# Kernel optimization log

Hardware: AMD Instinct MI355X
Metric: run time of the kernel (lower is better)

## Reference

```python
import jax, jax.numpy as jnp
import numpy as np
import math

B, N, DIM = 8, 4096, 768
H, D = 12, 64
STAGES = 3
LN_EPS = 1e-5

def _ln(x, g, b):
    mu = jnp.mean(x, axis=-1, keepdims=True)
    var = jnp.mean(jnp.square(x - mu), axis=-1, keepdims=True)
    return (x - mu) * jax.lax.rsqrt(var + LN_EPS) * g + b

def _mlp(x, W, b, g, be):
    return jax.nn.gelu(_ln(x @ W + b, g, be), approximate=False)

def setup_inputs() -> dict:
    key = jax.random.key(0)
    ks = jax.random.split(key, 16)
    s = lambda i, shape, sc: jax.random.normal(ks[i], shape, jnp.float32) * sc
    return {
        "x": s(0, (B, N, DIM), 1.0),
        "Wq": s(1, (DIM, H * D), DIM ** -0.5),
        "Wk": s(2, (DIM, H * D), DIM ** -0.5),
        "Wv": s(3, (DIM, H * D), DIM ** -0.5),
        "pool_W": s(4, (STAGES, D, D), D ** -0.5),
        "pool_b": jnp.zeros((STAGES, D), jnp.float32),
        "pool_g": jnp.ones((STAGES, D), jnp.float32),
        "pool_be": jnp.zeros((STAGES, D), jnp.float32),
        "exp_W": s(5, (STAGES, D, D), D ** -0.5),
        "exp_b": jnp.zeros((STAGES, D), jnp.float32),
        "exp_g": jnp.ones((STAGES, D), jnp.float32),
        "exp_be": jnp.zeros((STAGES, D), jnp.float32),
        "Wo": s(6, (H * D, DIM), (H * D) ** -0.5),
        "bo": jnp.zeros((DIM,), jnp.float32),
    }

def reference(x, Wq, Wk, Wv, pool_W, pool_b, pool_g, pool_be,
              exp_W, exp_b, exp_g, exp_be, Wo, bo):
    b, n, _ = x.shape
    # project and split heads -> (b, h, n, d)
    def heads(y):
        return y.reshape(b, n, H, D).transpose(0, 2, 1, 3)
    q = heads(x @ Wq)
    k = heads(x @ Wk)
    v = heads(x @ Wv)
    fmap = lambda t: jax.nn.elu(t) + 1.0
    q = fmap(q)
    k = fmap(k)

    kc, vc = k, v
    for i in range(STAGES):
        s = kc.shape[2]
        if s > 1:
            pad = (-s) % 2
            if pad:
                kc = jnp.pad(kc, ((0, 0), (0, 0), (0, pad), (0, 0)))
                vc = jnp.pad(vc, ((0, 0), (0, 0), (0, pad), (0, 0)))
            kc = kc.reshape(b, H, -1, 2, D).mean(axis=3)
            kc = _mlp(kc, pool_W[i], pool_b[i], pool_g[i], pool_be[i])
            vc = vc.reshape(b, H, -1, 2, D).mean(axis=3)

    kc = kc / math.sqrt(kc.shape[2])
    kv = jnp.einsum('bhnd,bhne->bhde', kc, vc)       # (b,h,d,d)
    out = jnp.einsum('bhnd,bhde->bhne', q, kv)       # (b,h,n,d)
    k_sum = kc.sum(axis=2, keepdims=True)            # (b,h,1,d)
    q_k_sum = jnp.sum(q * k_sum, axis=-1, keepdims=True)  # (b,h,n,1)
    out = out / (q_k_sum + 1e-6)

    for i in reversed(range(STAGES)):
        out = _mlp(out, exp_W[i], exp_b[i], exp_g[i], exp_be[i])

    out = out.transpose(0, 2, 1, 3).reshape(b, n, H * D)
    return out @ Wo + bo
```

## Files before the change

kernel.cpp:

```cpp
#include <hip/hip_runtime.h>
#include <math.h>

#define B_   8
#define N_   4096
#define DIM_ 768
#define H_   12
#define D_   64

typedef unsigned short ushort_t;
typedef unsigned int uint_t;
typedef __attribute__((ext_vector_type(8))) short short8;
typedef __attribute__((ext_vector_type(4))) float f32x4;

__device__ __forceinline__ float gelu_exact(float z) {
  const float ax = fabsf(z) * 0.70710678118654752440f;
  const float t  = __builtin_amdgcn_rcpf(1.f + 0.3275911f * ax);
  float poly = ((((1.061405429f * t - 1.453152027f) * t + 1.421413741f) * t
                 - 0.284496736f) * t + 0.254829592f) * t;
  const float erfax = 1.f - poly * __expf(-ax * ax);
  const float erfv = __builtin_copysignf(erfax, z);
  return 0.5f * z * (1.f + erfv);
}

__device__ __forceinline__ ushort_t f2bf(float f) {
  union { float f; unsigned u; } x; x.f = f;
  unsigned r = x.u + 0x7FFFu + ((x.u >> 16) & 1u);
  return (ushort_t)(r >> 16);
}

__device__ __forceinline__ float bf2f(ushort_t h) {
  union { unsigned u; float f; } x; x.u = ((unsigned)h) << 16;
  return x.f;
}

__device__ __forceinline__ void gl_lds16(const ushort_t* g, ushort_t* l) {
  __builtin_amdgcn_global_load_lds(
      (const __attribute__((address_space(1))) void*)g,
      (__attribute__((address_space(3))) void*)l, 16, 0, 0);
}

__global__ __launch_bounds__(256) void transpose_w_bf16(
    const float* __restrict__ src, ushort_t* __restrict__ dst)
{
  __shared__ float t[32][33];
  const int lx = threadIdx.x & 31, ly = threadIdx.x >> 5;
  const int bx = blockIdx.x * 32;
  const int by = blockIdx.y * 32;
  #pragma unroll
  for (int j = 0; j < 32; j += 8)
    t[ly + j][lx] = src[(size_t)(by + ly + j) * 768 + bx + lx];
  __syncthreads();
  #pragma unroll
  for (int j = 0; j < 32; j += 8)
    dst[(size_t)(bx + ly + j) * 768 + by + lx] = f2bf(t[lx][ly + j]);
}

__global__ __launch_bounds__(256) void transpose64_bf16(
    const float* __restrict__ pW, const float* __restrict__ eW,
    ushort_t* __restrict__ dst)
{
  const int m = blockIdx.x;
  const float* src = (m < 3) ? (pW + m * 4096) : (eW + (m - 3) * 4096);
  ushort_t* o = dst + m * 4096;
  for (int i = threadIdx.x; i < 4096; i += 256) {
    const int r = i >> 6, c = i & 63;
    o[c * 64 + r] = f2bf(src[r * 64 + c]);
  }
}

__global__ __launch_bounds__(256) void conv_f32_bf16(
    const float* __restrict__ src, ushort_t* __restrict__ dst)
{
  const int i = blockIdx.x * 256 + threadIdx.x;
  float4 f = ((const float4*)src)[i];
  ushort4 o;
  o.x = f2bf(f.x); o.y = f2bf(f.y); o.z = f2bf(f.z); o.w = f2bf(f.w);
  ((ushort4*)dst)[i] = o;
}

__global__ __launch_bounds__(256) void pool8_x(
    const ushort_t* __restrict__ xb, ushort_t* __restrict__ x8)
{
  const int idx = blockIdx.x * 256 + threadIdx.x;
  const int r = idx / 96, gc = idx - r * 96;
  const ushort_t* p = xb + (size_t)(8 * r) * 768 + gc * 8;
  float s[8] = {};
  #pragma unroll
  for (int j = 0; j < 8; ++j) {
    short8 v = *(const short8*)(p + (size_t)j * 768);
    #pragma unroll
    for (int e = 0; e < 8; ++e) s[e] += bf2f((ushort_t)v[e]);
  }
  short8 o;
  #pragma unroll
  for (int e = 0; e < 8; ++e) o[e] = (short)f2bf(0.125f * s[e]);
  *(short8*)(x8 + (size_t)r * 768 + gc * 8) = o;
}

#define GEMM_MAINLOOP(A, Bt, K)                                               \
  __shared__ ushort_t As[128 * 32];                                           \
  __shared__ ushort_t Bs[128 * 32];                                           \
  const int tid = threadIdx.x;                                                \
  const int nwg_ = (int)(gridDim.x * gridDim.y);                              \
  const int wgid0_ = (int)(blockIdx.y * gridDim.x + blockIdx.x);              \
  const int wgid_ = (wgid0_ & 7) * (nwg_ >> 3) + (wgid0_ >> 3);               \
  const int row0 = (wgid_ / (int)gridDim.x) * 128;                            \
  const int col0 = (wgid_ % (int)gridDim.x) * 128;                            \
  const int sr = tid >> 2;                                                    \
  const int sk = (tid & 3) * 8;                                               \
  const ushort_t* Ag0 = (A) + (size_t)(row0 + sr) * (K) + sk;                 \
  const ushort_t* Ag1 = Ag0 + (size_t)64 * (K);                               \
  const ushort_t* Bg0 = (Bt) + (size_t)(col0 + sr) * (K) + sk;                \
  const ushort_t* Bg1 = Bg0 + (size_t)64 * (K);                               \
  ushort_t* Asw = As + (tid >> 6) * 512;                                      \
  ushort_t* Bsw = Bs + (tid >> 6) * 512;                                      \
  const int w = tid >> 6, lane = tid & 63;                                    \
  const int wm = w >> 1, wn = w & 1;                                          \
  const int qd = lane >> 4, l15 = lane & 15;                                  \
  const int aoff = (wm * 64 + l15) * 32 + qd * 8;                             \
  const int boff = (wn * 64 + l15) * 32 + qd * 8;                             \
  f32x4 acc[4][4] = {};                                                       \
  for (int k0 = 0; k0 < (K); k0 += 32) {                                      \
    __syncthreads();                                                          \
    gl_lds16(Ag0 + k0, Asw);                                                  \
    gl_lds16(Ag1 + k0, Asw + 2048);                                           \
    gl_lds16(Bg0 + k0, Bsw);                                                  \
    gl_lds16(Bg1 + k0, Bsw + 2048);                                           \
    __syncthreads();                                                          \
    short8 af[4], bfr[4];                                                     \
    _Pragma("unroll")                                                         \
    for (int mt = 0; mt < 4; ++mt) af[mt] = *(const short8*)&As[aoff + mt * 512]; \
    _Pragma("unroll")                                                         \
    for (int nt = 0; nt < 4; ++nt) bfr[nt] = *(const short8*)&Bs[boff + nt * 512]; \
    _Pragma("unroll")                                                         \
    for (int mt = 0; mt < 4; ++mt)                                            \
      _Pragma("unroll")                                                       \
      for (int nt = 0; nt < 4; ++nt)                                          \
        acc[mt][nt] = __builtin_amdgcn_mfma_f32_16x16x32_bf16(                \
            af[mt], bfr[nt], acc[mt][nt], 0, 0, 0);                           \
  }

__global__ __launch_bounds__(256) void gemm_qkv(
    const ushort_t* __restrict__ A, const ushort_t* __restrict__ Bt,
    ushort_t* __restrict__ qo, ushort_t* __restrict__ ko)
{
  GEMM_MAINLOOP(A, Bt, 768)
  const int sel = col0 / 768;
  const int colbase = (col0 % 768) + wn * 64;
  ushort_t* o = (sel == 0) ? qo : ko;
  #pragma unroll
  for (int mt = 0; mt < 4; ++mt) {
    #pragma unroll
    for (int nt = 0; nt < 4; ++nt) {
      const int cg = colbase + nt * 16 + l15;
      #pragma unroll
      for (int r = 0; r < 4; ++r) {
        const int rg = row0 + wm * 64 + mt * 16 + qd * 4 + r;
        const float vv = acc[mt][nt][r];
        const float e = (vv > 0.f) ? vv + 1.f : __expf(vv);
        o[(size_t)rg * 768 + cg] = f2bf(e);
      }
    }
  }
}

__global__ __launch_bounds__(256) void gemm_v(
    const ushort_t* __restrict__ A, const ushort_t* __restrict__ Bt,
    float* __restrict__ vco)
{
  GEMM_MAINLOOP(A, Bt, 768)
  #pragma unroll
  for (int mt = 0; mt < 4; ++mt) {
    #pragma unroll
    for (int nt = 0; nt < 4; ++nt) {
      const int cg = col0 + wn * 64 + nt * 16 + l15;
      const int hh = cg >> 6, d = cg & 63;
      #pragma unroll
      for (int r = 0; r < 4; ++r) {
        const int rg = row0 + wm * 64 + mt * 16 + qd * 4 + r;
        const int b = rg >> 9, n = rg & 511;
        vco[(((size_t)b * 12 + hh) * 512 + n) * 64 + d] = acc[mt][nt][r];
      }
    }
  }
}

__global__ __launch_bounds__(256) void gemm_out(
    const ushort_t* __restrict__ A, const ushort_t* __restrict__ Bt,
    const float* __restrict__ bo, float* __restrict__ C)
{
  GEMM_MAINLOOP(A, Bt, 768)
  #pragma unroll
  for (int mt = 0; mt < 4; ++mt) {
    #pragma unroll
    for (int nt = 0; nt < 4; ++nt) {
      const int cg = col0 + wn * 64 + nt * 16 + l15;
      #pragma unroll
      for (int r = 0; r < 4; ++r) {
        const int rg = row0 + wm * 64 + mt * 16 + qd * 4 + r;
        C[(size_t)rg * 768 + cg] = acc[mt][nt][r] + bo[cg];
      }
    }
  }
}

__device__ __forceinline__ void mlp_stage(
    const ushort_t* __restrict__ inb, ushort_t* __restrict__ outb,
    const ushort_t* __restrict__ Wls, const float* __restrict__ bias,
    const float* __restrict__ g, const float* __restrict__ be,
    int rowbase, int ntiles, int tid)
{
  if (ntiles == 0) return;
  const int lane = tid & 63, quad = lane >> 4, l15 = lane & 15;
  float bv[4], gv[4], bev[4];
  #pragma unroll
  for (int nt = 0; nt < 4; ++nt) {
    const int c = nt * 16 + l15;
    bv[nt] = bias[c]; gv[nt] = g[c]; bev[nt] = be[c];
  }
  f32x4 a2[2][4];
  #pragma unroll
  for (int mt = 0; mt < 2; ++mt)
    #pragma unroll
    for (int nt = 0; nt < 4; ++nt)
      a2[mt][nt] = f32x4{bv[nt], bv[nt], bv[nt], bv[nt]};

  #pragma unroll
  for (int ks = 0; ks < 2; ++ks) {
    short8 af[2], bfr[4];
    #pragma unroll
    for (int mt = 0; mt < 2; ++mt)
      if (mt < ntiles)
        af[mt] = *(const short8*)&inb[(rowbase + mt * 16 + l15) * 72 + ks * 32 + quad * 8];
    #pragma unroll
    for (int nt = 0; nt < 4; ++nt)
      bfr[nt] = *(const short8*)&Wls[(nt * 16 + l15) * 72 + ks * 32 + quad * 8];
    #pragma unroll
    for (int mt = 0; mt < 2; ++mt)
      if (mt < ntiles)
        #pragma unroll
        for (int nt = 0; nt < 4; ++nt)
          a2[mt][nt] = __builtin_amdgcn_mfma_f32_16x16x32_bf16(af[mt], bfr[nt], a2[mt][nt], 0, 0, 0);
  }

  #pragma unroll
  for (int mt = 0; mt < 2; ++mt) {
    if (mt >= ntiles) continue;
    #pragma unroll
    for (int r = 0; r < 4; ++r) {
      float sum = a2[mt][0][r] + a2[mt][1][r] + a2[mt][2][r] + a2[mt][3][r];
      #pragma unroll
      for (int m = 1; m < 16; m <<= 1) sum += __shfl_xor(sum, m, 64);
      const float mu = sum * 0.015625f;
      float dv[4], var = 0.f;
      #pragma unroll
      for (int nt = 0; nt < 4; ++nt) { dv[nt] = a2[mt][nt][r] - mu; var += dv[nt] * dv[nt]; }
      #pragma unroll
      for (int m = 1; m < 16; m <<= 1) var += __shfl_xor(var, m, 64);
      const float rstd = rsqrtf(var * 0.015625f + 1e-5f);
      const int rl = rowbase + mt * 16 + quad * 4 + r;
      #pragma unroll
      for (int nt = 0; nt < 4; ++nt) {
        const float z = dv[nt] * rstd * gv[nt] + bev[nt];
        outb[rl * 72 + nt * 16 + l15] = f2bf(gelu_exact(z));
      }
    }
  }
}

__device__ __forceinline__ void pool_pairs(
    const ushort_t* __restrict__ inb, ushort_t* __restrict__ outb,
    int outRows, int tid)
{
  for (int idx = tid; idx < outRows * 8; idx += 256) {
    const int rl = idx >> 3, ch = idx & 7;
    short8 a = *(const short8*)&inb[(2 * rl) * 72 + ch * 8];
    short8 b = *(const short8*)&inb[(2 * rl + 1) * 72 + ch * 8];
    short8 o;
    #pragma unroll
    for (int e = 0; e < 8; ++e)
      o[e] = (short)f2bf(0.5f * (bf2f((ushort_t)a[e]) + bf2f((ushort_t)b[e])));
    *(short8*)&outb[rl * 72 + ch * 8] = o;
  }
}

__global__ __launch_bounds__(256) void pool_kv_fused(
    const ushort_t* __restrict__ k16, const float* __restrict__ vc,
    const ushort_t* __restrict__ pWt,
    const float* __restrict__ pb, const float* __restrict__ pg,
    const float* __restrict__ pbe,
    float* __restrict__ kvp, float* __restrict__ ksp)
{
  __shared__ ushort_t Wl[3 * 64 * 72];
  __shared__ ushort_t bufA[128 * 72];
  __shared__ ushort_t bufB[128 * 72];
  __shared__ float    vs[32 * 64];
  const int tid = threadIdx.x;
  const int x = blockIdx.x;
  const int h = blockIdx.y;
  const int bb = blockIdx.z;
  const ushort_t* kin = k16 + (size_t)bb * 3145728;
  const float* vp = vc + (size_t)bb * 393216 + ((size_t)h * 512 + x * 32) * 64;

  {
    const uint_t* ws = (const uint_t*)pWt;
    for (int i = tid; i < 6144; i += 256) {
      const int s = i >> 11, rem = i & 2047, r = rem >> 5, c = rem & 31;
      ((uint_t*)(Wl + (s * 64 + r) * 72))[c] = ws[i];
    }
  }
  #pragma unroll
  for (int j = 0; j < 4; ++j) {
    const int idx = j * 256 + tid;
    const int rl = idx >> 3, ch = idx & 7;
    const ushort_t* p = kin + (size_t)h * 64 + (size_t)(2 * (x * 128 + rl)) * 768 + ch * 8;
    short8 a = *(const short8*)p;
    short8 b2 = *(const short8*)(p + 768);
    short8 o;
    #pragma unroll
    for (int e = 0; e < 8; ++e)
      o[e] = (short)f2bf(0.5f * (bf2f((ushort_t)a[e]) + bf2f((ushort_t)b2[e])));
    *(short8*)&bufA[rl * 72 + ch * 8] = o;
  }
  #pragma unroll
  for (int i = 0; i < 2; ++i)
    ((float4*)vs)[tid + 256 * i] = ((const float4*)vp)[tid + 256 * i];
  __syncthreads();

  const int w = tid >> 6;
  mlp_stage(bufA, bufB, Wl, pb, pg, pbe, w * 32, 2, tid);
  __syncthreads();
  pool_pairs(bufB, bufA, 64, tid);
  __syncthreads();
  mlp_stage(bufA, bufB, Wl + 64 * 72, pb + 64, pg + 64, pbe + 64, w * 16, 1, tid);
  __syncthreads();
  pool_pairs(bufB, bufA, 32, tid);
  __syncthreads();
  mlp_stage(bufA, bufB, Wl + 128 * 72, pb + 128, pg + 128, pbe + 128,
            w * 16, (w < 2) ? 1 : 0, tid);
  __syncthreads();

  const int e = tid & 63;
  const int dg = tid >> 6;
  float acc[16] = {};
  float accs = 0.f;
  for (int nn = 0; nn < 32; ++nn) {
    const float vv = vs[nn * 64 + e];
    #pragma unroll
    for (int j = 0; j < 16; ++j)
      acc[j] += bf2f(bufB[nn * 72 + dg * 16 + j]) * vv;
    if (tid < 64) accs += bf2f(bufB[nn * 72 + tid]);
  }
  float* o = kvp + (size_t)bb * 786432 + ((size_t)h * 16 + x) * 4096;
  #pragma unroll
  for (int j = 0; j < 16; ++j)
    o[(dg * 16 + j) * 64 + e] = acc[j];
  if (tid < 64) ksp[(size_t)bb * 12288 + (h * 16 + x) * 64 + tid] = accs;
}

__global__ __launch_bounds__(256) void kv_reduce_t(
    const float* __restrict__ kvp, const float* __restrict__ ksp,
    ushort_t* __restrict__ kvxT)
{
  const int bb = blockIdx.y;
  kvp  += (size_t)bb * 786432;
  ksp  += (size_t)bb * 12288;
  kvxT += (size_t)bb * 61440;
  const int idx = blockIdx.x * 256 + threadIdx.x;
  const int h = idx / 5120;
  const int rem = idx - h * 5120;
  const int er = rem >> 6, d = rem & 63;
  const float scale = 0.044194173824159216f;
  float val = 0.f;
  if (er < 64) {
    float s = 0.f;
    #pragma unroll
    for (int c = 0; c < 16; ++c) s += kvp[((size_t)h * 16 + c) * 4096 + d * 64 + er];
    val = s * scale;
  } else if (er == 64) {
    float s = 0.f;
    #pragma unroll
    for (int c = 0; c < 16; ++c) s += ksp[(h * 16 + c) * 64 + d];
    val = s * scale;
  }
  kvxT[idx] = f2bf(val);
}

__global__ __launch_bounds__(256) void attn_exp_mfma(
    const ushort_t* __restrict__ q16, const ushort_t* __restrict__ kvxT,
    const ushort_t* __restrict__ eWt,
    const float* __restrict__ eb, const float* __restrict__ eg,
    const float* __restrict__ ebe, ushort_t* __restrict__ out16)
{
  __shared__ ushort_t Wl[3 * 64 * 72];
  __shared__ ushort_t tl[128 * 72];
  const int tid = threadIdx.x;
  const int h = blockIdx.y;
  const int bb = blockIdx.z;
  const int row0 = blockIdx.x * 128;
  q16   += (size_t)bb * 3145728;
  out16 += (size_t)bb * 3145728;
  const ushort_t* kvx = kvxT + (size_t)bb * 61440 + (size_t)h * 5120;

  {
    const uint_t* ws = (const uint_t*)eWt;
    for (int i = tid; i < 6144; i += 256) {
      const int s = i >> 11, rem = i & 2047, r = rem >> 5, c = rem & 31;
      ((uint_t*)(Wl + (s * 64 + r) * 72))[c] = ws[i];
    }
  }
  __syncthreads();

  const int w = tid >> 6, lane = tid & 63;
  const int quad = lane >> 4, l15 = lane & 15;

  f32x4 acc[2][5] = {};
  #pragma unroll
  for (int ks = 0; ks < 2; ++ks) {
    short8 af[2], bfr[5];
    #pragma unroll
    for (int mt = 0; mt < 2; ++mt) {
      const int rg = row0 + w * 32 + mt * 16 + l15;
      af[mt] = *(const short8*)(q16 + (size_t)rg * 768 + h * 64 + ks * 32 + quad * 8);
    }
    #pragma unroll
    for (int nt = 0; nt < 5; ++nt)
      bfr[nt] = *(const short8*)(kvx + (nt * 16 + l15) * 64 + ks * 32 + quad * 8);
    #pragma unroll
    for (int mt = 0; mt < 2; ++mt)
      #pragma unroll
      for (int nt = 0; nt < 5; ++nt)
        acc[mt][nt] = __builtin_amdgcn_mfma_f32_16x16x32_bf16(af[mt], bfr[nt], acc[mt][nt], 0, 0, 0);
  }

  float t[2][4][4];
  #pragma unroll
  for (int mt = 0; mt < 2; ++mt)
    #pragma unroll
    for (int r = 0; r < 4; ++r) {
      const float den = __shfl(acc[mt][4][r], lane & 48, 64) + 1e-6f;
      const float inv = __builtin_amdgcn_rcpf(den);
      #pragma unroll
      for (int nt = 0; nt < 4; ++nt)
        t[mt][nt][r] = acc[mt][nt][r] * inv;
    }

  for (int s = 2; s >= 0; --s) {
    __syncthreads();
    #pragma unroll
    for (int mt = 0; mt < 2; ++mt)
      #pragma unroll
      for (int nt = 0; nt < 4; ++nt)
        #pragma unroll
        for (int r = 0; r < 4; ++r)
          tl[(w * 32 + mt * 16 + quad * 4 + r) * 72 + nt * 16 + l15] = f2bf(t[mt][nt][r]);
    __syncthreads();

    float bv[4], gv[4], bev[4];
    #pragma unroll
    for (int nt = 0; nt < 4; ++nt) {
      const int c = s * 64 + nt * 16 + l15;
      bv[nt] = eb[c]; gv[nt] = eg[c]; bev[nt] = ebe[c];
    }
    f32x4 a2[2][4];
    #pragma unroll
    for (int mt = 0; mt < 2; ++mt)
      #pragma unroll
      for (int nt = 0; nt < 4; ++nt)
        a2[mt][nt] = f32x4{bv[nt], bv[nt], bv[nt], bv[nt]};

    #pragma unroll
    for (int ks = 0; ks < 2; ++ks) {
      short8 af[2], bfr[4];
      #pragma unroll
      for (int mt = 0; mt < 2; ++mt)
        af[mt] = *(const short8*)&tl[(w * 32 + mt * 16 + l15) * 72 + ks * 32 + quad * 8];
      #pragma unroll
      for (int nt = 0; nt < 4; ++nt)
        bfr[nt] = *(const short8*)&Wl[(s * 64 + nt * 16 + l15) * 72 + ks * 32 + quad * 8];
      #pragma unroll
      for (int mt = 0; mt < 2; ++mt)
        #pragma unroll
        for (int nt = 0; nt < 4; ++nt)
          a2[mt][nt] = __builtin_amdgcn_mfma_f32_16x16x32_bf16(af[mt], bfr[nt], a2[mt][nt], 0, 0, 0);
    }

    #pragma unroll
    for (int mt = 0; mt < 2; ++mt)
      #pragma unroll
      for (int r = 0; r < 4; ++r) {
        float sum = a2[mt][0][r] + a2[mt][1][r] + a2[mt][2][r] + a2[mt][3][r];
        #pragma unroll
        for (int m = 1; m < 16; m <<= 1) sum += __shfl_xor(sum, m, 64);
        const float mu = sum * 0.015625f;
        float dv[4], var = 0.f;
        #pragma unroll
        for (int nt = 0; nt < 4; ++nt) { dv[nt] = a2[mt][nt][r] - mu; var += dv[nt] * dv[nt]; }
        #pragma unroll
        for (int m = 1; m < 16; m <<= 1) var += __shfl_xor(var, m, 64);
        const float rstd = rsqrtf(var * 0.015625f + 1e-5f);
        #pragma unroll
        for (int nt = 0; nt < 4; ++nt) {
          const float z = dv[nt] * rstd * gv[nt] + bev[nt];
          t[mt][nt][r] = gelu_exact(z);
        }
      }
  }

  #pragma unroll
  for (int mt = 0; mt < 2; ++mt)
    #pragma unroll
    for (int nt = 0; nt < 4; ++nt)
      #pragma unroll
      for (int r = 0; r < 4; ++r) {
        const int rg = row0 + w * 32 + mt * 16 + quad * 4 + r;
        out16[(size_t)rg * 768 + h * 64 + nt * 16 + l15] = f2bf(t[mt][nt][r]);
      }
}

extern "C" void kernel_launch(void* const* d_in, const int* in_sizes, int n_in,
                              void* d_out, int out_size, void* d_ws, size_t ws_size,
                              hipStream_t stream)
{
  const float* x   = (const float*)d_in[0];
  const float* Wq  = (const float*)d_in[1];
  const float* Wk  = (const float*)d_in[2];
  const float* Wv  = (const float*)d_in[3];
  const float* pW  = (const float*)d_in[4];
  const float* pb  = (const float*)d_in[5];
  const float* pg  = (const float*)d_in[6];
  const float* pbe = (const float*)d_in[7];
  const float* eW  = (const float*)d_in[8];
  const float* eb  = (const float*)d_in[9];
  const float* eg  = (const float*)d_in[10];
  const float* ebe = (const float*)d_in[11];
  const float* Wo  = (const float*)d_in[12];
  const float* bo  = (const float*)d_in[13];
  float* outp = (float*)d_out;

  unsigned char* wsb = (unsigned char*)d_ws;
  ushort_t* WqkvT = (ushort_t*)(wsb + 0);
  ushort_t* WoT   = (ushort_t*)(wsb + 3538944);
  ushort_t* Wt6   = (ushort_t*)(wsb + 4718592);
  const size_t CB   = 4767744;
  const size_t PERB = 26861568;

  int NB;
  if      (ws_size >= CB + 8 * PERB) NB = 8;
  else if (ws_size >= CB + 4 * PERB) NB = 4;
  else if (ws_size >= CB + 2 * PERB) NB = 2;
  else if (ws_size >= CB + 1 * PERB) NB = 1;
  else return;

  unsigned char* cb = wsb + CB;
  ushort_t* xb16 = (ushort_t*)(cb);
  ushort_t* q16  = (ushort_t*)(cb + (size_t)NB *  6291456);
  ushort_t* k16  = (ushort_t*)(cb + (size_t)NB * 12582912);
  float*    vc   = (float*)   (cb + (size_t)NB * 18874368);
  ushort_t* kc_a = (ushort_t*)(cb + (size_t)NB * 20447232);
  ushort_t* kc_b = (ushort_t*)(cb + (size_t)NB * 23592960);
  ushort_t* kvxT = (ushort_t*)(cb + (size_t)NB * 25952256);
  ushort_t* x8   = (ushort_t*)(cb + (size_t)NB * 26075136);
  float* kvp = (float*)kc_a;
  float* ksp = (float*)kc_b;
  ushort_t* ao16 = xb16;

  const ushort_t* pWt = Wt6;
  const ushort_t* eWt = Wt6 + 3 * 4096;
  const size_t SB = (size_t)N_ * DIM_;

  transpose_w_bf16<<<dim3(24, 24), 256, 0, stream>>>(Wq, WqkvT);
  transpose_w_bf16<<<dim3(24, 24), 256, 0, stream>>>(Wk, WqkvT + 768 * 768);
  transpose_w_bf16<<<dim3(24, 24), 256, 0, stream>>>(Wv, WqkvT + 2 * 768 * 768);
  transpose_w_bf16<<<dim3(24, 24), 256, 0, stream>>>(Wo, WoT);
  transpose64_bf16<<<6, 256, 0, stream>>>(pW, eW, Wt6);

  const ushort_t* WvT = WqkvT + 2 * 768 * 768;

  for (int b0 = 0; b0 < B_; b0 += NB) {
    const float* xc = x + (size_t)b0 * SB;
    float* oc = outp + (size_t)b0 * SB;

    conv_f32_bf16<<<NB * 3072, 256, 0, stream>>>(xc, xb16);
    pool8_x<<<NB * 192, 256, 0, stream>>>(xb16, x8);
    gemm_qkv<<<dim3(12, NB * 32), 256, 0, stream>>>(xb16, WqkvT, q16, k16);
    gemm_v<<<dim3(6, NB * 4), 256, 0, stream>>>(x8, WvT, vc);

    pool_kv_fused<<<dim3(16, 12, NB), 256, 0, stream>>>(k16, vc, pWt,
                                                        pb, pg, pbe, kvp, ksp);
    kv_reduce_t<<<dim3(240, NB), 256, 0, stream>>>(kvp, ksp, kvxT);

    attn_exp_mfma<<<dim3(32, 12, NB), 256, 0, stream>>>(q16, kvxT, eWt,
                                                        eb, eg, ebe, ao16);

    gemm_out<<<dim3(6, NB * 32), 256, 0, stream>>>(ao16, WoT, bo, oc);
  }
}
```

Before: 581.3 us.

## Fuse bf16 conversion with 8-row pooling and double GEMM K-tile with XOR swizzle

The fp32-to-bf16 conversion and the 8-row mean pooling of x now run in one kernel, so x is read once and the bf16 copy is not re-read for pooling. The shared GEMM main loop now stages a K tile of 64 instead of 32, which halves the number of barrier pairs per GEMM. It also applies an XOR swizzle on the LDS layout to avoid bank conflicts. The larger tile doubles LDS use per block, which may reduce occupancy. Pooling now sums the fp32 values instead of bf16-rounded ones, which changes rounding slightly.

```diff
diff --git a/kernel.cpp b/kernel.cpp
--- a/kernel.cpp
+++ b/kernel.cpp
@@ -68,70 +68,76 @@
   }
 }
 
-__global__ __launch_bounds__(256) void conv_f32_bf16(
-    const float* __restrict__ src, ushort_t* __restrict__ dst)
-{
-  const int i = blockIdx.x * 256 + threadIdx.x;
-  float4 f = ((const float4*)src)[i];
-  ushort4 o;
-  o.x = f2bf(f.x); o.y = f2bf(f.y); o.z = f2bf(f.z); o.w = f2bf(f.w);
-  ((ushort4*)dst)[i] = o;
-}
-
-__global__ __launch_bounds__(256) void pool8_x(
-    const ushort_t* __restrict__ xb, ushort_t* __restrict__ x8)
-{
-  const int idx = blockIdx.x * 256 + threadIdx.x;
-  const int r = idx / 96, gc = idx - r * 96;
-  const ushort_t* p = xb + (size_t)(8 * r) * 768 + gc * 8;
-  float s[8] = {};
+__global__ __launch_bounds__(192) void conv_pool8(
+    const float* __restrict__ src, ushort_t* __restrict__ dst,
+    ushort_t* __restrict__ x8)
+{
+  const int g = blockIdx.x;
+  const int t = threadIdx.x;
+  const float4* s = (const float4*)(src + (size_t)g * 8 * 768);
+  ushort4* d = (ushort4*)(dst + (size_t)g * 8 * 768);
+  float4 sum = {0.f, 0.f, 0.f, 0.f};
   #pragma unroll
   for (int j = 0; j < 8; ++j) {
-    short8 v = *(const short8*)(p + (size_t)j * 768);
-    #pragma unroll
-    for (int e = 0; e < 8; ++e) s[e] += bf2f((ushort_t)v[e]);
-  }
-  short8 o;
-  #pragma unroll
-  for (int e = 0; e < 8; ++e) o[e] = (short)f2bf(0.125f * s[e]);
-  *(short8*)(x8 + (size_t)r * 768 + gc * 8) = o;
+    float4 f = s[j * 192 + t];
+    ushort4 o;
+    o.x = f2bf(f.x); o.y = f2bf(f.y); o.z = f2bf(f.z); o.w = f2bf(f.w);
+    d[j * 192 + t] = o;
+    sum.x += f.x; sum.y += f.y; sum.z += f.z; sum.w += f.w;
+  }
+  ushort4 m;
+  m.x = f2bf(0.125f * sum.x); m.y = f2bf(0.125f * sum.y);
+  m.z = f2bf(0.125f * sum.z); m.w = f2bf(0.125f * sum.w);
+  ((ushort4*)(x8 + (size_t)g * 768))[t] = m;
 }
 
 #define GEMM_MAINLOOP(A, Bt, K)                                               \
-  __shared__ ushort_t As[128 * 32];                                           \
-  __shared__ ushort_t Bs[128 * 32];                                           \
+  __shared__ ushort_t As[128 * 64];                                           \
+  __shared__ ushort_t Bs[128 * 64];                                           \
   const int tid = threadIdx.x;                                                \
   const int nwg_ = (int)(gridDim.x * gridDim.y);                              \
   const int wgid0_ = (int)(blockIdx.y * gridDim.x + blockIdx.x);              \
   const int wgid_ = (wgid0_ & 7) * (nwg_ >> 3) + (wgid0_ >> 3);               \
   const int row0 = (wgid_ / (int)gridDim.x) * 128;                            \
   const int col0 = (wgid_ % (int)gridDim.x) * 128;                            \
-  const int sr = tid >> 2;                                                    \
-  const int sk = (tid & 3) * 8;                                               \
-  const ushort_t* Ag0 = (A) + (size_t)(row0 + sr) * (K) + sk;                 \
-  const ushort_t* Ag1 = Ag0 + (size_t)64 * (K);                               \
-  const ushort_t* Bg0 = (Bt) + (size_t)(col0 + sr) * (K) + sk;                \
-  const ushort_t* Bg1 = Bg0 + (size_t)64 * (K);                               \
-  ushort_t* Asw = As + (tid >> 6) * 512;                                      \
-  ushort_t* Bsw = Bs + (tid >> 6) * 512;                                      \
+  const ushort_t* pA[4]; const ushort_t* pB[4];                               \
+  _Pragma("unroll")                                                           \
+  for (int j = 0; j < 4; ++j) {                                               \
+    const int g_ = tid + j * 256;                                             \
+    const int rr = g_ >> 3, sc = g_ & 7;                                      \
+    pA[j] = (A) + (size_t)(row0 + rr) * (K) + ((sc ^ (rr & 7)) << 3);         \
+    pB[j] = (Bt) + (size_t)(col0 + rr) * (K) + ((sc ^ (rr & 7)) << 3);        \
+  }                                                                           \
   const int w = tid >> 6, lane = tid & 63;                                    \
+  const int stw = w * 512;                                                    \
   const int wm = w >> 1, wn = w & 1;                                          \
   const int qd = lane >> 4, l15 = lane & 15;                                  \
-  const int aoff = (wm * 64 + l15) * 32 + qd * 8;                             \
-  const int boff = (wn * 64 + l15) * 32 + qd * 8;                             \
+  const int s0 = ((qd ^ (l15 & 7)) << 3);                                     \
+  const int abase = (wm * 64 + l15) * 64;                                     \
+  const int bbase = (wn * 64 + l15) * 64;                                     \
   f32x4 acc[4][4] = {};                                                       \
-  for (int k0 = 0; k0 < (K); k0 += 32) {                                      \
+  for (int k0 = 0; k0 < (K); k0 += 64) {                                      \
     __syncthreads();                                                          \
-    gl_lds16(Ag0 + k0, Asw);                                                  \
-    gl_lds16(Ag1 + k0, Asw + 2048);                                           \
-    gl_lds16(Bg0 + k0, Bsw);                                                  \
-    gl_lds16(Bg1 + k0, Bsw + 2048);                                           \
+    _Pragma("unroll")                                                         \
+    for (int j = 0; j < 4; ++j) gl_lds16(pA[j] + k0, As + j * 2048 + stw);    \
+    _Pragma("unroll")                                                         \
+    for (int j = 0; j < 4; ++j) gl_lds16(pB[j] + k0, Bs + j * 2048 + stw);    \
     __syncthreads();                                                          \
     short8 af[4], bfr[4];                                                     \
     _Pragma("unroll")                                                         \
-    for (int mt = 0; mt < 4; ++mt) af[mt] = *(const short8*)&As[aoff + mt * 512]; \
-    _Pragma("unroll")                                                         \
-    for (int nt = 0; nt < 4; ++nt) bfr[nt] = *(const short8*)&Bs[boff + nt * 512]; \
+    for (int mt = 0; mt < 4; ++mt) af[mt] = *(const short8*)&As[abase + mt * 1024 + s0]; \
+    _Pragma("unroll")                                                         \
+    for (int nt = 0; nt < 4; ++nt) bfr[nt] = *(const short8*)&Bs[bbase + nt * 1024 + s0]; \
+    _Pragma("unroll")                                                         \
+    for (int mt = 0; mt < 4; ++mt)                                            \
+      _Pragma("unroll")                                                       \
+      for (int nt = 0; nt < 4; ++nt)                                          \
+        acc[mt][nt] = __builtin_amdgcn_mfma_f32_16x16x32_bf16(                \
+            af[mt], bfr[nt], acc[mt][nt], 0, 0, 0);                           \
+    _Pragma("unroll")                                                         \
+    for (int mt = 0; mt < 4; ++mt) af[mt] = *(const short8*)&As[abase + mt * 1024 + (s0 ^ 32)]; \
+    _Pragma("unroll")                                                         \
+    for (int nt = 0; nt < 4; ++nt) bfr[nt] = *(const short8*)&Bs[bbase + nt * 1024 + (s0 ^ 32)]; \
     _Pragma("unroll")                                                         \
     for (int mt = 0; mt < 4; ++mt)                                            \
       _Pragma("unroll")                                                       \
@@ -581,8 +587,7 @@
     const float* xc = x + (size_t)b0 * SB;
     float* oc = outp + (size_t)b0 * SB;
 
-    conv_f32_bf16<<<NB * 3072, 256, 0, stream>>>(xc, xb16);
-    pool8_x<<<NB * 192, 256, 0, stream>>>(xb16, x8);
+    conv_pool8<<<NB * 512, 192, 0, stream>>>(xc, xb16, x8);
     gemm_qkv<<<dim3(12, NB * 32), 256, 0, stream>>>(xb16, WqkvT, q16, k16);
     gemm_v<<<dim3(6, NB * 4), 256, 0, stream>>>(x8, WvT, vc);
 
```

Result: faster. 566.6 us (-2.5%).
